# Performance work log

Measured on AMD Instinct MI355X. Metric: run time of the kernel, lower is better.

The kernel has to match this reference:

```python
import jax, jax.numpy as jnp
import numpy as np

EPS = 1e-6
H = 16  # num_heads

def _ln(x):
    mu = jnp.mean(x, axis=-1, keepdims=True)
    var = jnp.mean(jnp.square(x - mu), axis=-1, keepdims=True)
    return (x - mu) / jnp.sqrt(var + EPS)

def _mod(x, shift, scale):  # shift/scale: [B,D]
    return x * (1.0 + scale[:, None, :]) + shift[:, None, :]

def _heads(x, qkv_w, qkv_b):
    B, N, C = x.shape
    hd = C // H
    qkv = (x @ qkv_w + qkv_b).reshape(B, N, 3, H, hd).transpose(2, 0, 3, 1, 4)
    return qkv[0], qkv[1], qkv[2]  # each [B,H,N,hd]

def _attend(q, k, v):
    sc = (q.shape[-1]) ** -0.5
    a = jax.nn.softmax(jnp.einsum('bhnd,bhmd->bhnm', q, k) * sc, axis=-1)
    o = jnp.einsum('bhnm,bhmd->bhnd', a, v)
    B, h, N, hd = o.shape
    return o.transpose(0, 2, 1, 3).reshape(B, N, h * hd)

def _mha(x, qkv_w, qkv_b, proj_w, proj_b):
    q, k, v = _heads(x, qkv_w, qkv_b)
    return _attend(q, k, v) @ proj_w + proj_b

def setup_inputs() -> dict:
    key = jax.random.key(0)
    ks = jax.random.split(key, 16)
    B, T, D = 2, 2048, 1024
    Dh = 4 * D
    s = 0.02
    return {
        'x': jax.random.normal(ks[0], (B, T, D), jnp.float32),
        'c': jax.random.normal(ks[1], (B, 2, D), jnp.float32),
        'attn_qkv_w': jax.random.normal(ks[2], (D, 3 * D), jnp.float32) * s,
        'attn_qkv_b': jnp.zeros((3 * D,), jnp.float32),
        'attn_proj_w': jax.random.normal(ks[3], (D, D), jnp.float32) * s,
        'attn_proj_b': jnp.zeros((D,), jnp.float32),
        'crs_qkv_w': jax.random.normal(ks[4], (D, 3 * D), jnp.float32) * s,
        'crs_qkv_b': jnp.zeros((3 * D,), jnp.float32),
        'crs_proj_w': jax.random.normal(ks[5], (D, D), jnp.float32) * s,
        'crs_proj_b': jnp.zeros((D,), jnp.float32),
        'mlp_fc1_w': jax.random.normal(ks[6], (D, Dh), jnp.float32) * s,
        'mlp_fc1_b': jnp.zeros((Dh,), jnp.float32),
        'mlp_fc2_w': jax.random.normal(ks[7], (Dh, D), jnp.float32) * s,
        'mlp_fc2_b': jnp.zeros((D,), jnp.float32),
        'ada_w': jax.random.normal(ks[8], (D, 9 * D), jnp.float32) * s,
        'ada_b': jnp.zeros((9 * D,), jnp.float32),
    }

def reference(x, c, attn_qkv_w, attn_qkv_b, attn_proj_w, attn_proj_b,
              crs_qkv_w, crs_qkv_b, crs_proj_w, crs_proj_b,
              mlp_fc1_w, mlp_fc1_b, mlp_fc2_w, mlp_fc2_b, ada_w, ada_b):
    # adaLN-zero modulation: SiLU + Linear -> 9 chunks of [B,2,D]
    mod = jax.nn.silu(c) @ ada_w + ada_b
    (sh_msa, sc_msa, g_msa, sh_mca, sc_mca, g_mca,
     sh_mlp, sc_mlp, g_mlp) = jnp.split(mod, 9, axis=2)
    B, T, D = x.shape
    h = T // 2
    x0, x1 = x[:, :h], x[:, h:]
    # self-attention on each half with its own shift/scale/gate
    x0 = x0 + g_msa[:, 0][:, None, :] * _mha(_mod(_ln(x0), sh_msa[:, 0], sc_msa[:, 0]),
                                             attn_qkv_w, attn_qkv_b, attn_proj_w, attn_proj_b)
    x1 = x1 + g_msa[:, 1][:, None, :] * _mha(_mod(_ln(x1), sh_msa[:, 1], sc_msa[:, 1]),
                                             attn_qkv_w, attn_qkv_b, attn_proj_w, attn_proj_b)
    # two-way cross-attention
    xm = _mod(_ln(x0), sh_mca[:, 0], sc_mca[:, 0])
    ym = _mod(_ln(x1), sh_mca[:, 1], sc_mca[:, 1])
    qx, kx, vx = _heads(xm, crs_qkv_w, crs_qkv_b)
    qy, ky, vy = _heads(ym, crs_qkv_w, crs_qkv_b)
    ox = _attend(qx, ky, vy) @ crs_proj_w + crs_proj_b
    oy = _attend(qy, kx, vx) @ crs_proj_w + crs_proj_b
    x = x + jnp.concatenate((g_mca[:, 0][:, None, :] * ox,
                             g_mca[:, 1][:, None, :] * oy), axis=1)
    # gated MLP on each half
    def mlp(z):
        return jax.nn.gelu(z @ mlp_fc1_w + mlp_fc1_b, approximate=True) @ mlp_fc2_w + mlp_fc2_b
    m0 = mlp(_mod(_ln(x[:, :h]), sh_mlp[:, 0], sc_mlp[:, 0]))
    m1 = mlp(_mod(_ln(x[:, h:]), sh_mlp[:, 1], sc_mlp[:, 1]))
    x = x + jnp.concatenate((g_mlp[:, 0][:, None, :] * m0,
                             g_mlp[:, 1][:, None, :] * m1), axis=1)
    return x
```

## Files before the change

### kernel.cpp

```cpp
#include <hip/hip_runtime.h>
#include <hip/hip_bf16.h>

#define BB 2
#define TT 2048
#define DD 1024
#define NH 16
#define HALF 1024
#define DHID 4096
#define ND9 9216
#define ROWS (BB*TT)

using bf16 = __hip_bfloat16;
typedef short bf16x8 __attribute__((ext_vector_type(8)));
typedef float f32x4 __attribute__((ext_vector_type(4)));
typedef unsigned short u16;

__device__ __forceinline__ float bits2f(u16 b){ return __uint_as_float(((unsigned)b) << 16); }
__device__ __forceinline__ u16 fb(float v){
    unsigned u = __float_as_uint(v);
    u += 0x7fffu + ((u >> 16) & 1u);
    return (u16)(u >> 16);
}
__device__ __forceinline__ u16 fbh(float v){
    bf16 b = __float2bfloat16(v);
    return *(u16*)&b;
}
__device__ __forceinline__ float fexp2(float x){
#if __has_builtin(__builtin_amdgcn_exp2f)
    return __builtin_amdgcn_exp2f(x);
#else
    return exp2f(x);
#endif
}
__device__ __forceinline__ void gl_lds16(const u16* g, u16* l) {
    __builtin_amdgcn_global_load_lds(
        (const __attribute__((address_space(1))) unsigned int*)g,
        (__attribute__((address_space(3))) unsigned int*)l, 16, 0, 0);
}

__global__ void ada_part(const float* __restrict__ c, const float* __restrict__ ada_w,
                         float* __restrict__ part) {
    __shared__ float sc_[4][64];
    int s = blockIdx.y;
    int k0 = s * 64;
    int n0 = blockIdx.x * 1024 + threadIdx.x * 4;
    {
        int r = threadIdx.x >> 6, k = threadIdx.x & 63;
        float v = c[r*DD + k0 + k];
        sc_[r][k] = v / (1.f + __expf(-v));
    }
    __syncthreads();
    float4 a0 = {0,0,0,0}, a1 = {0,0,0,0}, a2 = {0,0,0,0}, a3 = {0,0,0,0};
    for (int k = 0; k < 64; ++k) {
        float4 wv = *(const float4*)&ada_w[(size_t)(k0 + k)*ND9 + n0];
        float s0 = sc_[0][k], s1 = sc_[1][k], s2 = sc_[2][k], s3 = sc_[3][k];
        a0.x += s0*wv.x; a0.y += s0*wv.y; a0.z += s0*wv.z; a0.w += s0*wv.w;
        a1.x += s1*wv.x; a1.y += s1*wv.y; a1.z += s1*wv.z; a1.w += s1*wv.w;
        a2.x += s2*wv.x; a2.y += s2*wv.y; a2.z += s2*wv.z; a2.w += s2*wv.w;
        a3.x += s3*wv.x; a3.y += s3*wv.y; a3.z += s3*wv.z; a3.w += s3*wv.w;
    }
    *(float4*)&part[((size_t)(s*4 + 0))*ND9 + n0] = a0;
    *(float4*)&part[((size_t)(s*4 + 1))*ND9 + n0] = a1;
    *(float4*)&part[((size_t)(s*4 + 2))*ND9 + n0] = a2;
    *(float4*)&part[((size_t)(s*4 + 3))*ND9 + n0] = a3;
}

__global__ void ada_reduce(const float* __restrict__ part, const float* __restrict__ ada_b,
                           float* __restrict__ mod) {
    int g = blockIdx.x * 1024 + threadIdx.x * 4;
    int r = g / ND9, n = g - r*ND9;
    float4 acc = *(const float4*)&ada_b[n];
    #pragma unroll
    for (int s = 0; s < 16; ++s) {
        float4 p = *(const float4*)&part[((size_t)(s*4 + r))*ND9 + n];
        acc.x += p.x; acc.y += p.y; acc.z += p.z; acc.w += p.w;
    }
    *(float4*)&mod[(size_t)r*ND9 + n] = acc;
}

__global__ void resid_ln(const float* __restrict__ src, const u16* __restrict__ gv,
                         const float* __restrict__ mod, int jshift, int jscale,
                         float* __restrict__ dstf, bf16* __restrict__ y) {
    int row = blockIdx.x;
    int b = row / TT, t = row % TT;
    int cz = (t >= HALF) ? 1 : 0;
    const float* mp = mod + (size_t)(b*2 + cz) * ND9;
    int tid = threadIdx.x;
    int w = tid >> 6, lane = tid & 63;
    int d0 = tid * 4;
    float4 s = *(const float4*)&src[(size_t)row*DD + d0];
    float v[4] = {s.x, s.y, s.z, s.w};
    if (gv) {
        ushort4 g = *(const ushort4*)&gv[(size_t)row*DD + d0];
        v[0] += bits2f(g.x); v[1] += bits2f(g.y); v[2] += bits2f(g.z); v[3] += bits2f(g.w);
    }
    if (dstf) *(float4*)&dstf[(size_t)row*DD + d0] = (float4){v[0], v[1], v[2], v[3]};
    float sum = v[0]+v[1]+v[2]+v[3];
    float ssq = v[0]*v[0]+v[1]*v[1]+v[2]*v[2]+v[3]*v[3];
    #pragma unroll
    for (int o = 32; o > 0; o >>= 1) {
        sum += __shfl_down(sum, o);
        ssq += __shfl_down(ssq, o);
    }
    __shared__ float wsum[4], wssq[4];
    if (lane == 0) { wsum[w] = sum; wssq[w] = ssq; }
    __syncthreads();
    float sall = (wsum[0]+wsum[1]) + (wsum[2]+wsum[3]);
    float qall = (wssq[0]+wssq[1]) + (wssq[2]+wssq[3]);
    float mean = sall * (1.f/DD);
    float var = qall * (1.f/DD) - mean*mean;
    float rstd = rsqrtf(var + 1e-6f);
    float4 sh = *(const float4*)&mp[jshift*DD + d0];
    float4 sc = *(const float4*)&mp[jscale*DD + d0];
    ushort4 o4;
    o4.x = fb((v[0]-mean)*rstd*(1.f+sc.x) + sh.x);
    o4.y = fb((v[1]-mean)*rstd*(1.f+sc.y) + sh.y);
    o4.z = fb((v[2]-mean)*rstd*(1.f+sc.z) + sh.z);
    o4.w = fb((v[3]-mean)*rstd*(1.f+sc.w) + sh.w);
    *(ushort4*)((u16*)y + (size_t)row*DD + d0) = o4;
}

__global__ void transpose_w(const float* __restrict__ W, u16* __restrict__ Wt, int K, int N) {
    __shared__ float T[32][33];
    int n0 = blockIdx.x * 32, k0 = blockIdx.y * 32;
    int lx = threadIdx.x & 31, ly = threadIdx.x >> 5;
    #pragma unroll
    for (int i = 0; i < 4; ++i)
        T[ly + i*8][lx] = W[(size_t)(k0 + ly + i*8)*N + n0 + lx];
    __syncthreads();
    #pragma unroll
    for (int i = 0; i < 4; ++i) {
        int n = ly + i*8;
        Wt[(size_t)(n0 + n)*K + k0 + lx] = fb(T[lx][n]);
    }
}

__global__ void vtrans(const u16* __restrict__ qkv, u16* __restrict__ vt) {
    __shared__ u16 T[64][72];
    int kt = blockIdx.y;
    int gh = blockIdx.x;
    int tid = threadIdx.x;
    int key = tid >> 2, c8 = (tid & 3) * 16;
    const u16* src = qkv + (size_t)((gh >> 4)*1024 + kt*64 + key)*3072 + 2048 + (gh & 15)*64 + c8;
    *(uint4*)&T[key][c8]     = *(const uint4*)src;
    *(uint4*)&T[key][c8 + 8] = *(const uint4*)(src + 8);
    __syncthreads();
    int d = tid >> 2, kc = (tid & 3) * 16;
    u16 tmp[16];
    #pragma unroll
    for (int i = 0; i < 16; ++i) tmp[i] = T[kc + i][d];
    u16* dst = vt + ((size_t)gh*64 + d)*1024 + kt*64 + kc;
    *(uint4*)&dst[0] = *(const uint4*)&tmp[0];
    *(uint4*)&dst[8] = *(const uint4*)&tmp[8];
}

__device__ __forceinline__ void epi_store(u16* out, int N, int mm, int n, float v,
                                          const float* mod, int jg, int epi) {
    if (epi == 0) {
        out[(size_t)mm*N + n] = fb(v);
    } else if (epi == 1) {
        float z = 0.7978845608028654f*(v + 0.044715f*v*v*v);
        out[(size_t)mm*N + n] = fb(v / (1.f + __expf(-2.f*z)));
    } else {
        int brow = mm / TT, tt2 = mm % TT;
        int cz = (tt2 >= HALF) ? 1 : 0;
        const float* mp = mod + (size_t)(brow*2 + cz)*ND9 + (size_t)jg*DD;
        if (epi == 3) {
            out[(size_t)mm*N + n] = fb(mp[n]*v);
        } else {
            float* of = (float*)out;
            size_t idx = (size_t)mm*N + n;
            of[idx] += mp[n]*v;
        }
    }
}

__global__ __launch_bounds__(256, 2) void gemm_mfma(
    const u16* __restrict__ A, const u16* __restrict__ Wt, const float* __restrict__ bias,
    u16* __restrict__ out, const float* __restrict__ mod, int jg,
    int K, int N, int epi)
{
    __shared__ u16 As[128*64];
    __shared__ u16 Bs[128*64];
    int tid = threadIdx.x;
    int w = tid >> 6, lane = tid & 63;
    int quad = lane >> 4, l16 = lane & 15;
    int m0 = blockIdx.y * 128;
    int n0 = blockIdx.x * 128;
    int wr = (w & 1) * 64, wc = (w >> 1) * 64;

    f32x4 acc[4][4];
    #pragma unroll
    for (int i = 0; i < 4; ++i)
        #pragma unroll
        for (int j = 0; j < 4; ++j) acc[i][j] = (f32x4){0.f,0.f,0.f,0.f};

    const u16* Ag = A + (size_t)m0 * K;
    const u16* Bg = Wt + (size_t)n0 * K;
    int srow = lane >> 3;
    int scol = (((lane & 7) ^ ((lane >> 3) & 7))) * 8;
    int xsw = (l16 & 7);

    for (int k0 = 0; k0 < K; k0 += 64) {
        #pragma unroll
        for (int c = 0; c < 4; ++c) {
            int ch = w*4 + c;
            gl_lds16(Ag + (size_t)(ch*8 + srow)*K + k0 + scol, As + ch*512);
            gl_lds16(Bg + (size_t)(ch*8 + srow)*K + k0 + scol, Bs + ch*512);
        }
        __syncthreads();
        #pragma unroll
        for (int kk = 0; kk < 2; ++kk) {
            int pc = ((kk*4 + quad) ^ xsw) * 8;
            bf16x8 af[4], bfr[4];
            #pragma unroll
            for (int i = 0; i < 4; ++i) af[i] = *(const bf16x8*)&As[(wr + i*16 + l16)*64 + pc];
            #pragma unroll
            for (int j = 0; j < 4; ++j) bfr[j] = *(const bf16x8*)&Bs[(wc + j*16 + l16)*64 + pc];
            #pragma unroll
            for (int i = 0; i < 4; ++i)
                #pragma unroll
                for (int j = 0; j < 4; ++j)
                    acc[i][j] = __builtin_amdgcn_mfma_f32_16x16x32_bf16(af[i], bfr[j], acc[i][j], 0, 0, 0);
        }
        __syncthreads();
    }

    #pragma unroll
    for (int i = 0; i < 4; ++i)
        #pragma unroll
        for (int r = 0; r < 4; ++r) {
            int mm = m0 + wr + i*16 + quad*4 + r;
            #pragma unroll
            for (int j = 0; j < 4; ++j) {
                int n = n0 + wc + j*16 + l16;
                epi_store(out, N, mm, n, acc[i][j][r] + bias[n], mod, jg, epi);
            }
        }
}

__global__ __launch_bounds__(256, 2) void gemm64_k128(
    const u16* __restrict__ A, const u16* __restrict__ Wt, const float* __restrict__ bias,
    u16* __restrict__ out, const float* __restrict__ mod, int jg,
    int K, int N, int epi)
{
    __shared__ u16 As[2*64*64];
    __shared__ u16 Bs[2*128*64];
    int tid = threadIdx.x;
    int w = tid >> 6, lane = tid & 63;
    int quad = lane >> 4, l16 = lane & 15;
    int m0 = blockIdx.y * 64;
    int n0 = blockIdx.x * 128;

    f32x4 acc[4][2];
    #pragma unroll
    for (int i = 0; i < 4; ++i)
        #pragma unroll
        for (int j = 0; j < 2; ++j) acc[i][j] = (f32x4){0.f,0.f,0.f,0.f};

    const u16* Ag = A + (size_t)m0 * K;
    const u16* Bg = Wt + (size_t)n0 * K;
    int srow = lane >> 3;
    int scol = (((lane & 7) ^ ((lane >> 3) & 7))) * 8;
    int xsw = (l16 & 7);

    for (int k0 = 0; k0 < K; k0 += 128) {
        #pragma unroll
        for (int h = 0; h < 2; ++h) {
            #pragma unroll
            for (int c = 0; c < 2; ++c) {
                int ch = w*2 + c;
                gl_lds16(Ag + (size_t)(ch*8 + srow)*K + k0 + h*64 + scol, As + h*4096 + ch*512);
            }
            #pragma unroll
            for (int c = 0; c < 4; ++c) {
                int ch = w*4 + c;
                gl_lds16(Bg + (size_t)(ch*8 + srow)*K + k0 + h*64 + scol, Bs + h*8192 + ch*512);
            }
        }
        __syncthreads();
        #pragma unroll
        for (int kk = 0; kk < 4; ++kk) {
            int hh = kk >> 1;
            int pc = (((kk & 1)*4 + quad) ^ xsw) * 8;
            bf16x8 af[4], bfr[2];
            #pragma unroll
            for (int i = 0; i < 4; ++i) af[i] = *(const bf16x8*)&As[hh*4096 + (i*16 + l16)*64 + pc];
            #pragma unroll
            for (int j = 0; j < 2; ++j) bfr[j] = *(const bf16x8*)&Bs[hh*8192 + (w*32 + j*16 + l16)*64 + pc];
            #pragma unroll
            for (int i = 0; i < 4; ++i)
                #pragma unroll
                for (int j = 0; j < 2; ++j)
                    acc[i][j] = __builtin_amdgcn_mfma_f32_16x16x32_bf16(af[i], bfr[j], acc[i][j], 0, 0, 0);
        }
        __syncthreads();
    }

    #pragma unroll
    for (int i = 0; i < 4; ++i)
        #pragma unroll
        for (int r = 0; r < 4; ++r) {
            int mm = m0 + i*16 + quad*4 + r;
            #pragma unroll
            for (int j = 0; j < 2; ++j) {
                int n = n0 + w*32 + j*16 + l16;
                epi_store(out, N, mm, n, acc[i][j][r] + bias[n], mod, jg, epi);
            }
        }
}

__global__ __launch_bounds__(256) void attn_mfma(const u16* __restrict__ qkv,
                                                 const u16* __restrict__ vt,
                                                 u16* __restrict__ attn_out, int kv_swap) {
    __shared__ u16 Ks[64][72];
    __shared__ u16 Vs[64][72];
    __shared__ u16 Ps[4][16][72];
    int head = blockIdx.x, qt = blockIdx.y, bh = blockIdx.z;
    int kvbh = kv_swap ? (bh ^ 1) : bh;
    int tid = threadIdx.x;
    int w = tid >> 6, lane = tid & 63;
    int quad = lane >> 4, l16 = lane & 15;
    int qrow0 = bh*1024 + qt*64 + w*16;

    const u16* qp = qkv + (size_t)(qrow0 + l16)*3072 + head*64;
    bf16x8 qa0 = *(const bf16x8*)(qp + quad*8);
    bf16x8 qa1 = *(const bf16x8*)(qp + 32 + quad*8);

    f32x4 oacc[4];
    #pragma unroll
    for (int i = 0; i < 4; ++i) oacc[i] = (f32x4){0.f,0.f,0.f,0.f};
    float mst = -3e38f, lst = 0.f;

    int skey = tid >> 2, sc8 = (tid & 3) * 16;
    const u16* kbase = qkv + (size_t)(kvbh*1024 + skey)*3072 + 1024 + head*64 + sc8;
    const u16* vbase = vt + ((size_t)(kvbh*16 + head)*64 + skey)*1024 + sc8;

    uint4 kr0 = *(const uint4*)kbase;
    uint4 kr1 = *(const uint4*)(kbase + 8);
    uint4 vr0 = *(const uint4*)vbase;
    uint4 vr1 = *(const uint4*)(vbase + 8);

    const float SSC = 0.125f * 1.4426950408889634f;
    for (int kt = 0; kt < 16; ++kt) {
        __syncthreads();
        *(uint4*)&Ks[skey][sc8]     = kr0;
        *(uint4*)&Ks[skey][sc8 + 8] = kr1;
        *(uint4*)&Vs[skey][sc8]     = vr0;
        *(uint4*)&Vs[skey][sc8 + 8] = vr1;
        __syncthreads();
        if (kt < 15) {
            const u16* kp = kbase + (size_t)(kt + 1)*64*3072;
            kr0 = *(const uint4*)kp;
            kr1 = *(const uint4*)(kp + 8);
            const u16* vp = vbase + (kt + 1)*64;
            vr0 = *(const uint4*)vp;
            vr1 = *(const uint4*)(vp + 8);
        }

        f32x4 sacc[4];
        #pragma unroll
        for (int nt = 0; nt < 4; ++nt) sacc[nt] = (f32x4){0.f,0.f,0.f,0.f};
        __builtin_amdgcn_s_setprio(1);
        #pragma unroll
        for (int nt = 0; nt < 4; ++nt) {
            bf16x8 kb0 = *(const bf16x8*)&Ks[nt*16 + l16][quad*8];
            bf16x8 kb1 = *(const bf16x8*)&Ks[nt*16 + l16][32 + quad*8];
            sacc[nt] = __builtin_amdgcn_mfma_f32_16x16x32_bf16(kb0, qa0, sacc[nt], 0, 0, 0);
            sacc[nt] = __builtin_amdgcn_mfma_f32_16x16x32_bf16(kb1, qa1, sacc[nt], 0, 0, 0);
        }
        __builtin_amdgcn_s_setprio(0);

        float sv[4][4];
        float tm = -3e38f;
        #pragma unroll
        for (int nt = 0; nt < 4; ++nt)
            #pragma unroll
            for (int r = 0; r < 4; ++r) {
                sv[nt][r] = sacc[nt][r] * SSC;
                tm = fmaxf(tm, sv[nt][r]);
            }
        tm = fmaxf(tm, __shfl_xor(tm, 16));
        tm = fmaxf(tm, __shfl_xor(tm, 32));
        if (!__all(tm <= mst + 11.5f)) {
            float mnew = fmaxf(mst, tm);
            float alpha = fexp2(mst - mnew);
            lst *= alpha;
            #pragma unroll
            for (int dt = 0; dt < 4; ++dt)
                #pragma unroll
                for (int r = 0; r < 4; ++r) oacc[dt][r] *= alpha;
            mst = mnew;
        }
        float ls = 0.f;
        #pragma unroll
        for (int nt = 0; nt < 4; ++nt) {
            float p0 = fexp2(sv[nt][0] - mst), p1 = fexp2(sv[nt][1] - mst);
            float p2 = fexp2(sv[nt][2] - mst), p3 = fexp2(sv[nt][3] - mst);
            ls += (p0 + p1) + (p2 + p3);
            ushort4 pk = {fbh(p0), fbh(p1), fbh(p2), fbh(p3)};
            *(ushort4*)&Ps[w][l16][nt*16 + quad*4] = pk;
        }
        ls += __shfl_xor(ls, 16);
        ls += __shfl_xor(ls, 32);
        lst += ls;

        bf16x8 pa0 = *(const bf16x8*)&Ps[w][l16][quad*8];
        bf16x8 pa1 = *(const bf16x8*)&Ps[w][l16][32 + quad*8];
        __builtin_amdgcn_s_setprio(1);
        #pragma unroll
        for (int dt = 0; dt < 4; ++dt) {
            bf16x8 vb0 = *(const bf16x8*)&Vs[dt*16 + l16][quad*8];
            bf16x8 vb1 = *(const bf16x8*)&Vs[dt*16 + l16][32 + quad*8];
            oacc[dt] = __builtin_amdgcn_mfma_f32_16x16x32_bf16(vb0, pa0, oacc[dt], 0, 0, 0);
            oacc[dt] = __builtin_amdgcn_mfma_f32_16x16x32_bf16(vb1, pa1, oacc[dt], 0, 0, 0);
        }
        __builtin_amdgcn_s_setprio(0);
    }
    float rl = 1.f / lst;
    #pragma unroll
    for (int dt = 0; dt < 4; ++dt) {
        ushort4 o4 = {fbh(oacc[dt][0]*rl), fbh(oacc[dt][1]*rl),
                      fbh(oacc[dt][2]*rl), fbh(oacc[dt][3]*rl)};
        *(ushort4*)&attn_out[(size_t)(qrow0 + l16)*DD + head*64 + dt*16 + quad*4] = o4;
    }
}

extern "C" void kernel_launch(void* const* d_in, const int* in_sizes, int n_in,
                              void* d_out, int out_size, void* d_ws, size_t ws_size,
                              hipStream_t stream) {
    const float* x          = (const float*)d_in[0];
    const float* c          = (const float*)d_in[1];
    const float* attn_qkv_w = (const float*)d_in[2];
    const float* attn_qkv_b = (const float*)d_in[3];
    const float* attn_proj_w= (const float*)d_in[4];
    const float* attn_proj_b= (const float*)d_in[5];
    const float* crs_qkv_w  = (const float*)d_in[6];
    const float* crs_qkv_b  = (const float*)d_in[7];
    const float* crs_proj_w = (const float*)d_in[8];
    const float* crs_proj_b = (const float*)d_in[9];
    const float* fc1_w      = (const float*)d_in[10];
    const float* fc1_b      = (const float*)d_in[11];
    const float* fc2_w      = (const float*)d_in[12];
    const float* fc2_b      = (const float*)d_in[13];
    const float* ada_w      = (const float*)d_in[14];
    const float* ada_b      = (const float*)d_in[15];
    float* out = (float*)d_out;

    char* ws = (char*)d_ws;
    float* mod = (float*)ws;
    char* R1   = ws + (256u<<10);
    char* Yr   = R1 + (16u<<20);
    char* AOr  = Yr + (8u<<20);
    char* BIGr = AOr + (8u<<20);

    u16*   wt_a  = (u16*)R1;
    u16*   vt    = (u16*)(R1 + (8u<<20));
    bf16*  y     = (bf16*)Yr;
    u16*   wt_p  = (u16*)Yr;
    u16*   attn_o= (u16*)AOr;
    u16*   big   = (u16*)BIGr;
    u16*   gvB   = (u16*)BIGr;
    u16*   hstage= (u16*)AOr;
    u16*   fc1_t = (u16*)R1;
    u16*   fc2_t = (u16*)(R1 + (8u<<20));
    float* apart = (float*)BIGr;

    ada_part<<<dim3(9, 16), 256, 0, stream>>>(c, ada_w, apart);
    ada_reduce<<<36, 256, 0, stream>>>(apart, ada_b, mod);

    transpose_w<<<dim3(3*DD/32, DD/32), 256, 0, stream>>>(attn_qkv_w, wt_a, DD, 3*DD);
    resid_ln<<<ROWS, 256, 0, stream>>>(x, nullptr, mod, 0, 1, out, y);
    gemm_mfma<<<dim3(3*DD/128, ROWS/128), 256, 0, stream>>>((const u16*)y, wt_a, attn_qkv_b,
                                                            big, nullptr, 0, DD, 3*DD, 0);
    vtrans<<<dim3(64, 16), 256, 0, stream>>>(big, vt);
    attn_mfma<<<dim3(NH, 16, 4), 256, 0, stream>>>(big, vt, attn_o, 0);
    transpose_w<<<dim3(DD/32, DD/32), 256, 0, stream>>>(attn_proj_w, wt_p, DD, DD);
    gemm64_k128<<<dim3(DD/128, ROWS/64), 256, 0, stream>>>(attn_o, wt_p, attn_proj_b,
                                                           gvB, mod, 2, DD, DD, 3);
    resid_ln<<<ROWS, 256, 0, stream>>>(out, gvB, mod, 3, 4, nullptr, y);

    transpose_w<<<dim3(3*DD/32, DD/32), 256, 0, stream>>>(crs_qkv_w, wt_a, DD, 3*DD);
    gemm_mfma<<<dim3(3*DD/128, ROWS/128), 256, 0, stream>>>((const u16*)y, wt_a, crs_qkv_b,
                                                            big, nullptr, 0, DD, 3*DD, 0);
    vtrans<<<dim3(64, 16), 256, 0, stream>>>(big, vt);
    attn_mfma<<<dim3(NH, 16, 4), 256, 0, stream>>>(big, vt, attn_o, 1);
    transpose_w<<<dim3(DD/32, DD/32), 256, 0, stream>>>(crs_proj_w, wt_p, DD, DD);
    gemm64_k128<<<dim3(DD/128, ROWS/64), 256, 0, stream>>>(attn_o, wt_p, crs_proj_b,
                                                           gvB, mod, 5, DD, DD, 3);
    resid_ln<<<ROWS, 256, 0, stream>>>(out, gvB, mod, 6, 7, out, y);

    transpose_w<<<dim3(DHID/32, DD/32), 256, 0, stream>>>(fc1_w, fc1_t, DD, DHID);
    transpose_w<<<dim3(DD/32, DHID/32), 256, 0, stream>>>(fc2_w, fc2_t, DHID, DD);
    gemm_mfma<<<dim3(DHID/128, ROWS/128), 256, 0, stream>>>((const u16*)y, fc1_t, fc1_b,
                                                            hstage, nullptr, 0, DD, DHID, 1);
    gemm64_k128<<<dim3(DD/128, ROWS/64), 256, 0, stream>>>(hstage, fc2_t, fc2_b,
                                                           (u16*)out, mod, 8, DHID, DD, 4);
}
```

Measured before the change: 539.1 us.

## Double-buffer LDS tiles in GEMMs to overlap global loads with MFMA

Adds double-buffered variants of the 128x128 and 64x128 MFMA GEMMs. They prefetch the next 64-wide K tile into the alternate LDS buffer while computing on the current one, with one barrier per step. The 64-row GEMM also swaps grid axes so consecutive blocks walk along M, which changes how the same weight columns are reused in L2. The fc1, fc2 and projection GEMMs now use these kernels; the change costs more LDS per block and could lower occupancy.

Result: no change. 542.2 us (+0.6%).

```diff
diff --git a/kernel.cpp b/kernel.cpp
--- a/kernel.cpp
+++ b/kernel.cpp
@@ -239,7 +239,87 @@
         }
 }
 
-__global__ __launch_bounds__(256, 2) void gemm64_k128(
+__global__ __launch_bounds__(256, 2) void gemm_mfma_db(
+    const u16* __restrict__ A, const u16* __restrict__ Wt, const float* __restrict__ bias,
+    u16* __restrict__ out, const float* __restrict__ mod, int jg,
+    int K, int N, int epi)
+{
+    __shared__ u16 As[2*128*64];
+    __shared__ u16 Bs[2*128*64];
+    int tid = threadIdx.x;
+    int w = tid >> 6, lane = tid & 63;
+    int quad = lane >> 4, l16 = lane & 15;
+    int m0 = blockIdx.y * 128;
+    int n0 = blockIdx.x * 128;
+    int wr = (w & 1) * 64, wc = (w >> 1) * 64;
+
+    f32x4 acc[4][4];
+    #pragma unroll
+    for (int i = 0; i < 4; ++i)
+        #pragma unroll
+        for (int j = 0; j < 4; ++j) acc[i][j] = (f32x4){0.f,0.f,0.f,0.f};
+
+    const u16* Ag = A + (size_t)m0 * K;
+    const u16* Bg = Wt + (size_t)n0 * K;
+    int srow = lane >> 3;
+    int scol = (((lane & 7) ^ ((lane >> 3) & 7))) * 8;
+    int xsw = (l16 & 7);
+
+    #pragma unroll
+    for (int c = 0; c < 4; ++c) {
+        int ch = w*4 + c;
+        gl_lds16(Ag + (size_t)(ch*8 + srow)*K + scol, As + ch*512);
+        gl_lds16(Bg + (size_t)(ch*8 + srow)*K + scol, Bs + ch*512);
+    }
+    asm volatile("s_waitcnt vmcnt(0)" ::: "memory");
+    __builtin_amdgcn_s_barrier();
+
+    int NT = K >> 6;
+    int cur = 0;
+    for (int t = 0; t < NT; ++t) {
+        if (t + 1 < NT) {
+            int k1 = (t + 1) << 6;
+            int nb = cur ^ 1;
+            #pragma unroll
+            for (int c = 0; c < 4; ++c) {
+                int ch = w*4 + c;
+                gl_lds16(Ag + (size_t)(ch*8 + srow)*K + k1 + scol, As + nb*8192 + ch*512);
+                gl_lds16(Bg + (size_t)(ch*8 + srow)*K + k1 + scol, Bs + nb*8192 + ch*512);
+            }
+        }
+        #pragma unroll
+        for (int kk = 0; kk < 2; ++kk) {
+            int pc = ((kk*4 + quad) ^ xsw) * 8;
+            bf16x8 af[4], bfr[4];
+            #pragma unroll
+            for (int i = 0; i < 4; ++i) af[i] = *(const bf16x8*)&As[cur*8192 + (wr + i*16 + l16)*64 + pc];
+            #pragma unroll
+            for (int j = 0; j < 4; ++j) bfr[j] = *(const bf16x8*)&Bs[cur*8192 + (wc + j*16 + l16)*64 + pc];
+            #pragma unroll
+            for (int i = 0; i < 4; ++i)
+                #pragma unroll
+                for (int j = 0; j < 4; ++j)
+                    acc[i][j] = __builtin_amdgcn_mfma_f32_16x16x32_bf16(af[i], bfr[j], acc[i][j], 0, 0, 0);
+        }
+        asm volatile("s_waitcnt vmcnt(0)" ::: "memory");
+        __builtin_amdgcn_s_barrier();
+        cur ^= 1;
+    }
+
+    #pragma unroll
+    for (int i = 0; i < 4; ++i)
+        #pragma unroll
+        for (int r = 0; r < 4; ++r) {
+            int mm = m0 + wr + i*16 + quad*4 + r;
+            #pragma unroll
+            for (int j = 0; j < 4; ++j) {
+                int n = n0 + wc + j*16 + l16;
+                epi_store(out, N, mm, n, acc[i][j][r] + bias[n], mod, jg, epi);
+            }
+        }
+}
+
+__global__ __launch_bounds__(256, 2) void gemm64_db(
     const u16* __restrict__ A, const u16* __restrict__ Wt, const float* __restrict__ bias,
     u16* __restrict__ out, const float* __restrict__ mod, int jg,
     int K, int N, int epi)
@@ -249,8 +329,8 @@
     int tid = threadIdx.x;
     int w = tid >> 6, lane = tid & 63;
     int quad = lane >> 4, l16 = lane & 15;
-    int m0 = blockIdx.y * 64;
-    int n0 = blockIdx.x * 128;
+    int m0 = blockIdx.x * 64;
+    int n0 = blockIdx.y * 128;
 
     f32x4 acc[4][2];
     #pragma unroll
@@ -264,37 +344,53 @@
     int scol = (((lane & 7) ^ ((lane >> 3) & 7))) * 8;
     int xsw = (l16 & 7);
 
-    for (int k0 = 0; k0 < K; k0 += 128) {
-        #pragma unroll
-        for (int h = 0; h < 2; ++h) {
+    #pragma unroll
+    for (int c = 0; c < 2; ++c) {
+        int ch = w*2 + c;
+        gl_lds16(Ag + (size_t)(ch*8 + srow)*K + scol, As + ch*512);
+    }
+    #pragma unroll
+    for (int c = 0; c < 4; ++c) {
+        int ch = w*4 + c;
+        gl_lds16(Bg + (size_t)(ch*8 + srow)*K + scol, Bs + ch*512);
+    }
+    asm volatile("s_waitcnt vmcnt(0)" ::: "memory");
+    __builtin_amdgcn_s_barrier();
+
+    int NT = K >> 6;
+    int cur = 0;
+    for (int t = 0; t < NT; ++t) {
+        if (t + 1 < NT) {
+            int k1 = (t + 1) << 6;
+            int nb = cur ^ 1;
             #pragma unroll
             for (int c = 0; c < 2; ++c) {
                 int ch = w*2 + c;
-                gl_lds16(Ag + (size_t)(ch*8 + srow)*K + k0 + h*64 + scol, As + h*4096 + ch*512);
+                gl_lds16(Ag + (size_t)(ch*8 + srow)*K + k1 + scol, As + nb*4096 + ch*512);
             }
             #pragma unroll
             for (int c = 0; c < 4; ++c) {
                 int ch = w*4 + c;
-                gl_lds16(Bg + (size_t)(ch*8 + srow)*K + k0 + h*64 + scol, Bs + h*8192 + ch*512);
-            }
-        }
-        __syncthreads();
-        #pragma unroll
-        for (int kk = 0; kk < 4; ++kk) {
-            int hh = kk >> 1;
-            int pc = (((kk & 1)*4 + quad) ^ xsw) * 8;
+                gl_lds16(Bg + (size_t)(ch*8 + srow)*K + k1 + scol, Bs + nb*8192 + ch*512);
+            }
+        }
+        #pragma unroll
+        for (int kk = 0; kk < 2; ++kk) {
+            int pc = ((kk*4 + quad) ^ xsw) * 8;
             bf16x8 af[4], bfr[2];
             #pragma unroll
-            for (int i = 0; i < 4; ++i) af[i] = *(const bf16x8*)&As[hh*4096 + (i*16 + l16)*64 + pc];
-            #pragma unroll
-            for (int j = 0; j < 2; ++j) bfr[j] = *(const bf16x8*)&Bs[hh*8192 + (w*32 + j*16 + l16)*64 + pc];
+            for (int i = 0; i < 4; ++i) af[i] = *(const bf16x8*)&As[cur*4096 + (i*16 + l16)*64 + pc];
+            #pragma unroll
+            for (int j = 0; j < 2; ++j) bfr[j] = *(const bf16x8*)&Bs[cur*8192 + (w*32 + j*16 + l16)*64 + pc];
             #pragma unroll
             for (int i = 0; i < 4; ++i)
                 #pragma unroll
                 for (int j = 0; j < 2; ++j)
                     acc[i][j] = __builtin_amdgcn_mfma_f32_16x16x32_bf16(af[i], bfr[j], acc[i][j], 0, 0, 0);
         }
-        __syncthreads();
+        asm volatile("s_waitcnt vmcnt(0)" ::: "memory");
+        __builtin_amdgcn_s_barrier();
+        cur ^= 1;
     }
 
     #pragma unroll
@@ -476,8 +572,8 @@
     vtrans<<<dim3(64, 16), 256, 0, stream>>>(big, vt);
     attn_mfma<<<dim3(NH, 16, 4), 256, 0, stream>>>(big, vt, attn_o, 0);
     transpose_w<<<dim3(DD/32, DD/32), 256, 0, stream>>>(attn_proj_w, wt_p, DD, DD);
-    gemm64_k128<<<dim3(DD/128, ROWS/64), 256, 0, stream>>>(attn_o, wt_p, attn_proj_b,
-                                                           gvB, mod, 2, DD, DD, 3);
+    gemm64_db<<<dim3(ROWS/64, DD/128), 256, 0, stream>>>(attn_o, wt_p, attn_proj_b,
+                                                         gvB, mod, 2, DD, DD, 3);
     resid_ln<<<ROWS, 256, 0, stream>>>(out, gvB, mod, 3, 4, nullptr, y);
 
     transpose_w<<<dim3(3*DD/32, DD/32), 256, 0, stream>>>(crs_qkv_w, wt_a, DD, 3*DD);
@@ -486,14 +582,14 @@
     vtrans<<<dim3(64, 16), 256, 0, stream>>>(big, vt);
     attn_mfma<<<dim3(NH, 16, 4), 256, 0, stream>>>(big, vt, attn_o, 1);
     transpose_w<<<dim3(DD/32, DD/32), 256, 0, stream>>>(crs_proj_w, wt_p, DD, DD);
-    gemm64_k128<<<dim3(DD/128, ROWS/64), 256, 0, stream>>>(attn_o, wt_p, crs_proj_b,
-                                                           gvB, mod, 5, DD, DD, 3);
+    gemm64_db<<<dim3(ROWS/64, DD/128), 256, 0, stream>>>(attn_o, wt_p, crs_proj_b,
+                                                         gvB, mod, 5, DD, DD, 3);
     resid_ln<<<ROWS, 256, 0, stream>>>(out, gvB, mod, 6, 7, out, y);
 
     transpose_w<<<dim3(DHID/32, DD/32), 256, 0, stream>>>(fc1_w, fc1_t, DD, DHID);
     transpose_w<<<dim3(DD/32, DHID/32), 256, 0, stream>>>(fc2_w, fc2_t, DHID, DD);
-    gemm_mfma<<<dim3(DHID/128, ROWS/128), 256, 0, stream>>>((const u16*)y, fc1_t, fc1_b,
-                                                            hstage, nullptr, 0, DD, DHID, 1);
-    gemm64_k128<<<dim3(DD/128, ROWS/64), 256, 0, stream>>>(hstage, fc2_t, fc2_b,
-                                                           (u16*)out, mod, 8, DHID, DD, 4);
-}
+    gemm_mfma_db<<<dim3(DHID/128, ROWS/128), 256, 0, stream>>>((const u16*)y, fc1_t, fc1_b,
+                                                               hstage, nullptr, 0, DD, DHID, 1);
+    gemm64_db<<<dim3(ROWS/64, DD/128), 256, 0, stream>>>(hstage, fc2_t, fc2_b,
+                                                         (u16*)out, mod, 8, DHID, DD, 4);
+}
```
